# Optimization experiments

Hardware: AMD Instinct MI355X
Metric: run time of the kernel (lower is better)

Reference implementation:

```python
import jax, jax.numpy as jnp
import numpy as np

B, F, T, D = 65536, 1024, 64, 6


def setup_inputs() -> dict:
    key = jax.random.key(0)
    k0, k1, k2, k3 = jax.random.split(key, 4)
    x = jax.random.normal(k0, (B, F), dtype=jnp.float32)
    splits = jax.random.normal(k1, (T, D, F), dtype=jnp.float32)
    thresholds = jax.random.normal(k2, (T, D), dtype=jnp.float32)
    values = jax.random.normal(k3, (T, 2 ** D), dtype=jnp.float32)
    return {"x": x, "splits": splits, "thresholds": thresholds, "values": values}


def reference(x, splits, thresholds, values):
    # Since split_idx = depth % max_depth = depth, each level's split is path-independent.
    # bit_d = 1 means 'right' (score > threshold); node after D steps = 2^D - 1 + code,
    # leaf_idx = node - 2^D = code - 1 (torch negative indexing => mod 2^D).
    T_, D_, _ = splits.shape
    scores = jnp.einsum('bf,tdf->tbd', x, splits)          # (T, B, D)
    bits = (scores > thresholds[:, None, :]).astype(jnp.int32)
    pow2 = (2 ** jnp.arange(D_ - 1, -1, -1)).astype(jnp.int32)  # weight 2^(D-1-d)
    code = jnp.sum(bits * pow2, axis=-1)                   # (T, B)
    leaf = jnp.mod(code - 1, 2 ** D_)                      # (T, B)
    out_t = jnp.take_along_axis(values, leaf, axis=1)      # (T, B)
    return jnp.mean(out_t, axis=0)[:, None]                # (B, 1)
```

## Files before the change

kernel.cpp:

```cpp
#include <hip/hip_runtime.h>

#define BTOT 65536
#define FDIM 1024
#define TNUM 64
#define DNUM 6

#define BAND      1.5e-3f
#define GCUT      1.5e-4f
#define HEDGE_MAX 1.35f
#define CAP       8192

typedef unsigned int u32;
typedef unsigned long long u64;
using f32x4  = __attribute__((ext_vector_type(4))) float;
using bf16x8 = __attribute__((ext_vector_type(8))) short;

__device__ __forceinline__ short f32_to_bf16(float v) {
    u32 bits = __float_as_uint(v);
    bits += 0x7FFFu + ((bits >> 16) & 1u);
    return (short)(bits >> 16);
}
__device__ __forceinline__ float bf16_to_f32(short h) {
    return __uint_as_float(((u32)(unsigned short)h) << 16);
}
__device__ __forceinline__ void cvt8(float4 a0, float4 a1, bf16x8& h, bf16x8& l) {
    const float vv[8] = {a0.x, a0.y, a0.z, a0.w, a1.x, a1.y, a1.z, a1.w};
    #pragma unroll
    for (int e = 0; e < 8; ++e) {
        const short hh = f32_to_bf16(vv[e]);
        h[e] = hh;
        l[e] = f32_to_bf16(vv[e] - bf16_to_f32(hh));
    }
}

__device__ __forceinline__ int swz(int row, int chunk) {
    return row * 32 + ((chunk ^ ((row >> 1) & 3)) << 3);
}
__device__ __forceinline__ int swzA(int row, int chunk) {
    return row * 32 + ((chunk ^ (row & 3)) << 3);
}

#define PRE_OFFSET  65536
#define BTILE_BYTES 24576
#define PRE_BYTES   (64 * BTILE_BYTES)
#define B_LO_OFF    6144
#define A_LO_SH     4096

#define LDS_BYTES 81920

__global__ void pre_split(const float* __restrict__ splits,
                          short* __restrict__ pre) {
    const int q  = blockIdx.x * 256 + threadIdx.x;
    const int r  = q >> 8;
    const int c4 = q & 255;
    const float4 v = *(const float4*)(splits + (size_t)r * FDIM + c4 * 4);
    const int ks    = c4 >> 3;
    const int f4    = c4 & 7;
    const int chunk = f4 >> 1, he = f4 & 1;
    const int h  = (r >= 192) ? 1 : 0;
    const int rl = r - h * 192;
    short* tile = pre + (size_t)(ks * 2 + h) * (BTILE_BYTES / 2);
    const int idx = swz(rl, chunk) + he * 4;
    const float vv[4] = {v.x, v.y, v.z, v.w};
    short hh[4], ll[4];
    #pragma unroll
    for (int e = 0; e < 4; ++e) {
        hh[e] = f32_to_bf16(vv[e]);
        ll[e] = f32_to_bf16(vv[e] - bf16_to_f32(hh[e]));
    }
    *(short4*)(tile + idx)            = make_short4(hh[0], hh[1], hh[2], hh[3]);
    *(short4*)(tile + B_LO_OFF + idx) = make_short4(ll[0], ll[1], ll[2], ll[3]);
}

__global__ __launch_bounds__(512, 4)
void forest_mfma(const float* __restrict__ x,
                 const float* __restrict__ thresholds,
                 const float* __restrict__ values,
                 float* __restrict__ out,
                 u32* __restrict__ gcnt,
                 u32* __restrict__ cands,
                 const short* __restrict__ pre) {
    __shared__ __align__(16) char smem[LDS_BYTES];

    const int tid  = threadIdx.x;
    const int lane = tid & 63;
    const int w    = tid >> 6;
    const int wr   = w >> 2;
    const int wc   = w & 3;
    const int fr   = lane & 15;
    const int fq   = lane >> 4;
    const int nb   = blockIdx.x >> 1;
    const int half = blockIdx.x & 1;
    const int b0   = nb * 128;

    const int arow = tid >> 2;
    const int ac   = tid & 3;
    const float* axp = x + (size_t)(b0 + arow) * FDIM + ac * 8;

    f32x4 acc[3][4];
    #pragma unroll
    for (int tt = 0; tt < 3; ++tt)
        #pragma unroll
        for (int bt = 0; bt < 4; ++bt) acc[tt][bt] = (f32x4)0.0f;

    auto stageB = [&](int ks, char* dstb) {
        const char* srcb = (const char*)pre + (size_t)(ks * 2 + half) * BTILE_BYTES;
        #pragma unroll
        for (int j = 0; j < 3; ++j) {
            const int cb = (j * 512 + w * 64) * 16;
            __builtin_amdgcn_global_load_lds(
                (const void*)(srcb + cb + (lane << 4)),
                (void*)(dstb + cb), 16, 0, 0);
        }
    };
    auto cvtwrA = [&](float4 p0, float4 p1, short* Adst) {
        bf16x8 h, l;
        cvt8(p0, p1, h, l);
        const int off = swzA(arow, ac);
        *(bf16x8*)(Adst + off)           = h;
        *(bf16x8*)(Adst + A_LO_SH + off) = l;
    };

    {
        float4 p0 = *(const float4*)(axp);
        float4 p1 = *(const float4*)(axp + 4);
        cvtwrA(p0, p1, (short*)smem);
    }
    stageB(0, smem + 32768);
    __syncthreads();

    float4 pa0, pa1;
    for (int ks = 0; ks < 32; ++ks) {
        const int cur = ks & 1;
        if (ks < 31) {
            pa0 = *(const float4*)(axp + (ks + 1) * 32);
            pa1 = *(const float4*)(axp + (ks + 1) * 32 + 4);
            stageB(ks + 1, smem + 32768 + (cur ^ 1) * 24576);
        }

        const short* As = (const short*)(smem + cur * 16384);
        const short* Bs = (const short*)(smem + 32768 + cur * 24576);

        bf16x8 sh[3], sl[3], xh[4], xl[4];
        #pragma unroll
        for (int tt = 0; tt < 3; ++tt) {
            const int row = wc * 48 + tt * 16 + fr;
            const int ix = swz(row, fq);
            sh[tt] = *(const bf16x8*)(Bs + ix);
            sl[tt] = *(const bf16x8*)(Bs + B_LO_OFF + ix);
        }
        #pragma unroll
        for (int bt = 0; bt < 4; ++bt) {
            const int row = wr * 64 + bt * 16 + fr;
            const int ix = swzA(row, fq);
            xh[bt] = *(const bf16x8*)(As + ix);
            xl[bt] = *(const bf16x8*)(As + A_LO_SH + ix);
        }

        __builtin_amdgcn_s_setprio(1);
        #pragma unroll
        for (int bt = 0; bt < 4; ++bt)
            #pragma unroll
            for (int tt = 0; tt < 3; ++tt) {
                acc[tt][bt] = __builtin_amdgcn_mfma_f32_16x16x32_bf16(sh[tt], xh[bt], acc[tt][bt], 0, 0, 0);
                acc[tt][bt] = __builtin_amdgcn_mfma_f32_16x16x32_bf16(sh[tt], xl[bt], acc[tt][bt], 0, 0, 0);
                acc[tt][bt] = __builtin_amdgcn_mfma_f32_16x16x32_bf16(sl[tt], xh[bt], acc[tt][bt], 0, 0, 0);
            }
        __builtin_amdgcn_s_setprio(0);

        if (ks < 31)
            cvtwrA(pa0, pa1, (short*)(smem + (cur ^ 1) * 16384));

        __syncthreads();
    }

    float th[3][4];
    #pragma unroll
    for (int tt = 0; tt < 3; ++tt)
        #pragma unroll
        for (int reg = 0; reg < 4; ++reg)
            th[tt][reg] = thresholds[half * 192 + wc * 48 + tt * 16 + fq * 4 + reg];

    float* psum = (float*)smem;

    #pragma unroll
    for (int bt = 0; bt < 4; ++bt) {
        u64 bal[3][4];
        u32 bandmask = 0;
        #pragma unroll
        for (int tt = 0; tt < 3; ++tt)
            #pragma unroll
            for (int reg = 0; reg < 4; ++reg) {
                const float df = acc[tt][bt][reg] - th[tt][reg];
                bal[tt][reg] = __ballot(df > 0.0f);
                if (__builtin_expect(fabsf(df) < BAND, 0))
                    bandmask |= 1u << ((tt * 16 + fq * 4 + reg) / 6);
            }
        bandmask |= __shfl_xor(bandmask, 16);
        bandmask |= __shfl_xor(bandmask, 32);

        float partial = 0.0f;
        #pragma unroll
        for (int jj = 0; jj < 2; ++jj) {
            const int j = fq * 2 + jj;
            int code = 0;
            #pragma unroll
            for (int d = 0; d < DNUM; ++d) {
                const int l   = j * 6 + d;
                const int stt = l >> 4;
                const int pos = l & 15;
                const int bit = (int)((bal[stt][pos & 3] >> (((pos >> 2) << 4) + fr)) & 1ull);
                code |= bit << (5 - d);
            }
            const int t = half * 32 + wc * 8 + j;
            partial += values[t * 64 + ((code - 1) & 63)];
            if (__builtin_expect((bandmask >> j) & 1u, 0)) {
                const u32 gidx = atomicAdd(gcnt, 1u);
                if (gidx < CAP)
                    cands[gidx] = ((u32)(b0 + wr * 64 + bt * 16 + fr) << 16) | ((u32)t << 6) | (u32)code;
            }
        }
        psum[(wr * 64 + bt * 16 + fr) * 16 + wc * 4 + fq] = partial;
    }
    __syncthreads();
    if (tid < 128) {
        float s = 0.0f;
        #pragma unroll
        for (int k = 0; k < 16; ++k) s += psum[tid * 16 + k];
        atomicAdd(out + b0 + tid, s * (1.0f / 64.0f));
    }
}

#define RPITCH 40
#define A_HI_S 0
#define A_LO_S (64 * RPITCH)
#define B_HI_S (128 * RPITCH)
#define B_LO_S (128 * RPITCH + 384 * RPITCH)
#define SMEM_SHORTS (128 * RPITCH + 2 * 384 * RPITCH)
__global__ __launch_bounds__(256, 2)
void forest_mfma_lds(const float* __restrict__ x,
                     const float* __restrict__ splits,
                     const float* __restrict__ thresholds,
                     const float* __restrict__ values,
                     float* __restrict__ out,
                     u32* __restrict__ gcnt,
                     u32* __restrict__ cands) {
    __shared__ __align__(16) short smem[SMEM_SHORTS];
    const int tid  = threadIdx.x;
    const int lane = tid & 63;
    const int w    = tid >> 6;
    const int fr   = lane & 15;
    const int fq   = lane >> 4;
    const int b0   = blockIdx.x * 64;

    f32x4 acc[6][4];
    #pragma unroll
    for (int tt = 0; tt < 6; ++tt)
        #pragma unroll
        for (int bt = 0; bt < 4; ++bt) acc[tt][bt] = (f32x4)0.0f;

    for (int ks = 0; ks < 32; ++ks) {
        const int k0 = ks * 32;
        if (ks) __syncthreads();
        #pragma unroll
        for (int j = 0; j < 2; ++j) {
            const int q = tid + j * 256, ra = q >> 3, c4 = q & 7;
            const float4 v = *(const float4*)(x + (size_t)(b0 + ra) * FDIM + k0 + c4 * 4);
            const float vv[4] = {v.x, v.y, v.z, v.w};
            short hh[4], ll[4];
            #pragma unroll
            for (int e = 0; e < 4; ++e) {
                hh[e] = f32_to_bf16(vv[e]);
                ll[e] = f32_to_bf16(vv[e] - bf16_to_f32(hh[e]));
            }
            *(short4*)(smem + A_HI_S + ra * RPITCH + c4 * 4) = make_short4(hh[0], hh[1], hh[2], hh[3]);
            *(short4*)(smem + A_LO_S + ra * RPITCH + c4 * 4) = make_short4(ll[0], ll[1], ll[2], ll[3]);
        }
        #pragma unroll
        for (int j = 0; j < 12; ++j) {
            const int q = tid + j * 256, rb = q >> 3, c4 = q & 7;
            const float4 v = *(const float4*)(splits + (size_t)rb * FDIM + k0 + c4 * 4);
            const float vv[4] = {v.x, v.y, v.z, v.w};
            short hh[4], ll[4];
            #pragma unroll
            for (int e = 0; e < 4; ++e) {
                hh[e] = f32_to_bf16(vv[e]);
                ll[e] = f32_to_bf16(vv[e] - bf16_to_f32(hh[e]));
            }
            *(short4*)(smem + B_HI_S + rb * RPITCH + c4 * 4) = make_short4(hh[0], hh[1], hh[2], hh[3]);
            *(short4*)(smem + B_LO_S + rb * RPITCH + c4 * 4) = make_short4(ll[0], ll[1], ll[2], ll[3]);
        }
        __syncthreads();
        bf16x8 sh[6], sl[6], xh[4], xl[4];
        #pragma unroll
        for (int tt = 0; tt < 6; ++tt) {
            const int ro = (w * 96 + tt * 16 + fr) * RPITCH + fq * 8;
            sh[tt] = *(const bf16x8*)(smem + B_HI_S + ro);
            sl[tt] = *(const bf16x8*)(smem + B_LO_S + ro);
        }
        #pragma unroll
        for (int bt = 0; bt < 4; ++bt) {
            const int ro = (bt * 16 + fr) * RPITCH + fq * 8;
            xh[bt] = *(const bf16x8*)(smem + A_HI_S + ro);
            xl[bt] = *(const bf16x8*)(smem + A_LO_S + ro);
        }
        #pragma unroll
        for (int tt = 0; tt < 6; ++tt)
            #pragma unroll
            for (int bt = 0; bt < 4; ++bt) {
                acc[tt][bt] = __builtin_amdgcn_mfma_f32_16x16x32_bf16(sh[tt], xh[bt], acc[tt][bt], 0, 0, 0);
                acc[tt][bt] = __builtin_amdgcn_mfma_f32_16x16x32_bf16(sh[tt], xl[bt], acc[tt][bt], 0, 0, 0);
                acc[tt][bt] = __builtin_amdgcn_mfma_f32_16x16x32_bf16(sl[tt], xh[bt], acc[tt][bt], 0, 0, 0);
            }
    }
    __syncthreads();

    float th[6][4];
    #pragma unroll
    for (int tt = 0; tt < 6; ++tt)
        #pragma unroll
        for (int reg = 0; reg < 4; ++reg)
            th[tt][reg] = thresholds[w * 96 + tt * 16 + fq * 4 + reg];
    float* psum = (float*)smem;
    __syncthreads();
    #pragma unroll
    for (int bt = 0; bt < 4; ++bt) {
        u64 bal[6][4];
        u32 bandmask = 0;
        #pragma unroll
        for (int tt = 0; tt < 6; ++tt)
            #pragma unroll
            for (int reg = 0; reg < 4; ++reg) {
                const float df = acc[tt][bt][reg] - th[tt][reg];
                bal[tt][reg] = __ballot(df > 0.0f);
                if (__builtin_expect(fabsf(df) < BAND, 0))
                    bandmask |= 1u << ((tt * 16 + fq * 4 + reg) / 6);
            }
        bandmask |= __shfl_xor(bandmask, 16);
        bandmask |= __shfl_xor(bandmask, 32);
        float partial = 0.0f;
        #pragma unroll
        for (int jj = 0; jj < 4; ++jj) {
            const int j = fq * 4 + jj;
            int code = 0;
            #pragma unroll
            for (int d = 0; d < DNUM; ++d) {
                const int l   = j * 6 + d;
                const int stt = l >> 4;
                const int pos = l & 15;
                const int bit = (int)((bal[stt][pos & 3] >> (((pos >> 2) << 4) + fr)) & 1ull);
                code |= bit << (5 - d);
            }
            const int t = w * 16 + j;
            partial += values[t * 64 + ((code - 1) & 63)];
            if (__builtin_expect((bandmask >> j) & 1u, 0)) {
                const u32 gidx = atomicAdd(gcnt, 1u);
                if (gidx < CAP)
                    cands[gidx] = ((u32)(b0 + bt * 16 + fr) << 16) | ((u32)t << 6) | (u32)code;
            }
        }
        psum[(bt * 16 + fr) * 16 + w * 4 + fq] = partial;
    }
    __syncthreads();
    if (tid < 64) {
        float s = 0.0f;
        #pragma unroll
        for (int k = 0; k < 16; ++k) s += psum[tid * 16 + k];
        out[b0 + tid] = s * (1.0f / 64.0f);
    }
}

__global__ __launch_bounds__(256)
void band_fix(const float* __restrict__ x,
              const float* __restrict__ splits,
              const float* __restrict__ thresholds,
              const float* __restrict__ values,
              float* __restrict__ out,
              const u32* __restrict__ gcnt,
              const u32* __restrict__ cands) {
    const u32 n = min(*gcnt, (u32)CAP);
    const u32 gid  = blockIdx.x * 256 + threadIdx.x;
    const u32 site = gid >> 3;
    const u32 sub  = gid & 7;
    if (site >= n) return;
    const u32 e = cands[site];
    const int b = (int)(e >> 16);
    const int t = (int)((e >> 6) & 63u);
    const int code_approx = (int)(e & 63u);
    const int d = (sub < 6) ? (int)sub : 0;

    const float* xr = x + (size_t)b * FDIM;
    const float* sr = splits + ((size_t)t * DNUM + d) * FDIM;
    float a = 0.0f;
    #pragma unroll 4
    for (int f = 0; f < FDIM; f += 16) {
        const float4 x0 = *(const float4*)(xr + f);
        const float4 x1 = *(const float4*)(xr + f + 4);
        const float4 x2 = *(const float4*)(xr + f + 8);
        const float4 x3 = *(const float4*)(xr + f + 12);
        const float4 s0 = *(const float4*)(sr + f);
        const float4 s1 = *(const float4*)(sr + f + 4);
        const float4 s2 = *(const float4*)(sr + f + 8);
        const float4 s3 = *(const float4*)(sr + f + 12);
        a = fmaf(x0.x, s0.x, a); a = fmaf(x0.y, s0.y, a);
        a = fmaf(x0.z, s0.z, a); a = fmaf(x0.w, s0.w, a);
        a = fmaf(x1.x, s1.x, a); a = fmaf(x1.y, s1.y, a);
        a = fmaf(x1.z, s1.z, a); a = fmaf(x1.w, s1.w, a);
        a = fmaf(x2.x, s2.x, a); a = fmaf(x2.y, s2.y, a);
        a = fmaf(x2.z, s2.z, a); a = fmaf(x2.w, s2.w, a);
        a = fmaf(x3.x, s3.x, a); a = fmaf(x3.y, s3.y, a);
        a = fmaf(x3.z, s3.z, a); a = fmaf(x3.w, s3.w, a);
    }
    const float df = a - thresholds[t * DNUM + d];

    const int lane = (int)(threadIdx.x & 63);
    const int base = lane & ~7;
    float dfs[6];
    #pragma unroll
    for (int j = 0; j < 6; ++j) dfs[j] = __shfl(df, base + j);

    if (sub == 0) {
        int code_chain = 0;
        #pragma unroll
        for (int j = 0; j < 6; ++j)
            code_chain = (code_chain << 1) | (dfs[j] > 0.0f ? 1 : 0);
        const float vA = values[t * 64 + ((code_approx - 1) & 63)];
        const float vC = values[t * 64 + ((code_chain - 1) & 63)];
        float delta = vC - vA;
        #pragma unroll
        for (int j = 0; j < 6; ++j) {
            if (fabsf(dfs[j]) < GCUT) {
                const int cf = code_chain ^ (1 << (5 - j));
                const float dv = values[t * 64 + ((cf - 1) & 63)] - vC;
                if (fabsf(dv) < HEDGE_MAX) delta += dv * 0.5f;
            }
        }
        atomicAdd(out + b, delta * (1.0f / 64.0f));
    }
}

extern "C" void kernel_launch(void* const* d_in, const int* in_sizes, int n_in,
                              void* d_out, int out_size, void* d_ws, size_t ws_size,
                              hipStream_t stream) {
    const float* x          = (const float*)d_in[0];
    const float* splits     = (const float*)d_in[1];
    const float* thresholds = (const float*)d_in[2];
    const float* values     = (const float*)d_in[3];
    float* out = (float*)d_out;

    u32* gcnt   = (u32*)d_ws;
    u32* cands  = (u32*)((char*)d_ws + 64);
    short* pre  = (short*)((char*)d_ws + PRE_OFFSET);
    const int use_pre = (ws_size >= (size_t)PRE_OFFSET + (size_t)PRE_BYTES) ? 1 : 0;

    (void)hipMemsetAsync(gcnt, 0, 4, stream);
    if (use_pre) {
        (void)hipMemsetAsync(d_out, 0, (size_t)out_size * sizeof(float), stream);
        pre_split<<<dim3(384), dim3(256), 0, stream>>>(splits, pre);
        forest_mfma<<<dim3((BTOT / 128) * 2), dim3(512), 0, stream>>>(
            x, thresholds, values, out, gcnt, cands, pre);
    } else {
        forest_mfma_lds<<<dim3(BTOT / 64), dim3(256), 0, stream>>>(
            x, splits, thresholds, values, out, gcnt, cands);
    }
    band_fix<<<dim3(CAP * 8 / 256), dim3(256), 0, stream>>>(
        x, splits, thresholds, values, out, gcnt, cands);
}
```

Before: 223.2 us.

## Prefetch x two k-steps ahead with fine-grained waitcnt and XCD-aware block mapping

The main loop now loads the x tile two k-steps ahead into alternating register sets. It replaces __syncthreads with an explicit s_waitcnt vmcnt(2) plus s_barrier, so the next step's global loads can stay in flight across the barrier, and sched_barriers keep the compiler from reordering the loads. Block indices are also remapped so that consecutive blocks on the same XCD work on different row tiles while both halves of a tile share an XCD, which is meant to improve L2 locality for x. The cost is more registers live for the extra prefetch, and correctness now depends on the hand-counted vmcnt values.

```diff
diff --git a/kernel.cpp b/kernel.cpp
--- a/kernel.cpp
+++ b/kernel.cpp
@@ -45,8 +45,7 @@
 #define PRE_BYTES   (64 * BTILE_BYTES)
 #define B_LO_OFF    6144
 #define A_LO_SH     4096
-
-#define LDS_BYTES 81920
+#define LDS_BYTES   81920
 
 __global__ void pre_split(const float* __restrict__ splits,
                           short* __restrict__ pre) {
@@ -89,8 +88,10 @@
     const int wc   = w & 3;
     const int fr   = lane & 15;
     const int fq   = lane >> 4;
-    const int nb   = blockIdx.x >> 1;
-    const int half = blockIdx.x & 1;
+    const int bid  = blockIdx.x;
+    const int xcd  = bid & 7;
+    const int half = (bid >> 3) & 1;
+    const int nb   = (bid >> 4) * 8 + xcd;
     const int b0   = nb * 128;
 
     const int arow = tid >> 2;
@@ -121,22 +122,17 @@
         *(bf16x8*)(Adst + A_LO_SH + off) = l;
     };
 
-    {
-        float4 p0 = *(const float4*)(axp);
-        float4 p1 = *(const float4*)(axp + 4);
-        cvtwrA(p0, p1, (short*)smem);
-    }
-    stageB(0, smem + 32768);
-    __syncthreads();
-
-    float4 pa0, pa1;
-    for (int ks = 0; ks < 32; ++ks) {
+    auto kstep = [&](int ks, float4& pi0, float4& pi1,
+                     float4& pc0, float4& pc1) {
         const int cur = ks & 1;
-        if (ks < 31) {
-            pa0 = *(const float4*)(axp + (ks + 1) * 32);
-            pa1 = *(const float4*)(axp + (ks + 1) * 32 + 4);
+        if (ks < 31)
             stageB(ks + 1, smem + 32768 + (cur ^ 1) * 24576);
-        }
+        __builtin_amdgcn_sched_barrier(0);
+        if (ks < 30) {
+            pi0 = *(const float4*)(axp + (ks + 2) * 32);
+            pi1 = *(const float4*)(axp + (ks + 2) * 32 + 4);
+        }
+        __builtin_amdgcn_sched_barrier(0);
 
         const short* As = (const short*)(smem + cur * 16384);
         const short* Bs = (const short*)(smem + 32768 + cur * 24576);
@@ -169,10 +165,37 @@
         __builtin_amdgcn_s_setprio(0);
 
         if (ks < 31)
-            cvtwrA(pa0, pa1, (short*)(smem + (cur ^ 1) * 16384));
-
-        __syncthreads();
-    }
+            cvtwrA(pc0, pc1, (short*)(smem + (cur ^ 1) * 16384));
+
+        if (ks < 31) {
+            if (ks < 30) asm volatile("s_waitcnt vmcnt(2) lgkmcnt(0)" ::: "memory");
+            else         asm volatile("s_waitcnt vmcnt(0) lgkmcnt(0)" ::: "memory");
+            __builtin_amdgcn_s_barrier();
+            __builtin_amdgcn_sched_barrier(0);
+        }
+    };
+
+    float4 paA0, paA1, paB0, paB1;
+    {
+        float4 a0 = *(const float4*)(axp);
+        float4 a1 = *(const float4*)(axp + 4);
+        stageB(0, smem + 32768);
+        __builtin_amdgcn_sched_barrier(0);
+        paA0 = *(const float4*)(axp + 32);
+        paA1 = *(const float4*)(axp + 32 + 4);
+        __builtin_amdgcn_sched_barrier(0);
+        cvtwrA(a0, a1, (short*)smem);
+        asm volatile("s_waitcnt vmcnt(2) lgkmcnt(0)" ::: "memory");
+        __builtin_amdgcn_s_barrier();
+        __builtin_amdgcn_sched_barrier(0);
+    }
+
+    #pragma unroll 1
+    for (int kk = 0; kk < 16; ++kk) {
+        kstep(2 * kk,     paB0, paB1, paA0, paA1);
+        kstep(2 * kk + 1, paA0, paA1, paB0, paB1);
+    }
+    __syncthreads();
 
     float th[3][4];
     #pragma unroll
```

Result: slower. 258.4 us (+15.8%).
